# Optimization experiments

Hardware: AMD Instinct MI355X
Metric: run time of the kernel (lower is better)

The kernel has to match this reference:

```python
import jax, jax.numpy as jnp
import numpy as np

NUM_HEADS = 8


def setup_inputs() -> dict:
    key = jax.random.key(0)
    ks = jax.random.split(key, 7)
    B, D, N = 16, 512, 2048
    sc = 1.0 / np.sqrt(D)
    return {
        "X_Query": jax.random.normal(ks[0], (B, D, N), jnp.float32),
        "X_Key": jax.random.normal(ks[1], (B, D, N), jnp.float32),
        "X_Value": jax.random.normal(ks[2], (B, D, N), jnp.float32),
        "W_q": jax.random.normal(ks[3], (D, D), jnp.float32) * sc,
        "W_k": jax.random.normal(ks[4], (D, D), jnp.float32) * sc,
        "W_v": jax.random.normal(ks[5], (D, D), jnp.float32) * sc,
        "W_o": jax.random.normal(ks[6], (D, D), jnp.float32) * sc,
    }


def _proj(W, x):
    # Conv1d(D, D, kernel_size=1, bias=False) == channel matmul
    return jnp.einsum('oi,bin->bon', W, x)


def _split_heads(x, h):
    # torch: cat(x.chunk(h, dim=-1), dim=0) -> (h, B, D, N/h) stacked layout
    B, D, N = x.shape
    return x.reshape(B, D, h, N // h).transpose(2, 0, 1, 3)


def _mha(XQ, XK, XV, Wq, Wk, Wv, Wo):
    B, D, N = XQ.shape
    h = NUM_HEADS
    Nh = N // h
    q = _split_heads(_proj(Wq, XQ), h)  # (h, B, D, Nh)
    k = _split_heads(_proj(Wk, XK), h)
    v = _split_heads(_proj(Wv, XV), h)
    # scores over the CHANNEL axis: (h, B, D, D), scaled by sqrt(d_k)=sqrt(Nh)
    scores = jnp.einsum('hbdn,hben->hbde', q, k) / jnp.sqrt(jnp.asarray(Nh, q.dtype))
    p = jax.nn.softmax(scores, axis=-1)
    out = jnp.einsum('hbde,hben->hbdn', p, v)  # (h, B, D, Nh)
    # torch: cat(chunks, dim=0) inverse -> cat along dim=-1
    attn_heads = out.transpose(1, 2, 0, 3).reshape(B, D, N)
    return _proj(Wo, XQ - attn_heads)


def reference(X_Query, X_Key, X_Value, W_q, W_k, W_v, W_o):
    return _mha(X_Query, X_Key, X_Value, W_q, W_k, W_v, W_o)
```

## Files before the change

kernel.cpp:

```cpp
#include <hip/hip_runtime.h>
#include <hip/hip_bf16.h>

#define DD  512
#define NN  2048
#define BB  16
#define NHD 256

typedef unsigned short u16;
typedef __attribute__((ext_vector_type(4))) float f32x4;
typedef __attribute__((ext_vector_type(8))) short s16x8;
typedef __attribute__((ext_vector_type(4))) u16   u16x4;

static __device__ __forceinline__ u16 f2bf(float f) {
  __hip_bfloat16 h = __float2bfloat16(f);
  return *reinterpret_cast<u16*>(&h);
}
static __device__ __forceinline__ float bf2f(u16 u) {
  union { unsigned int i; float f; } v; v.i = ((unsigned int)u) << 16; return v.f;
}
static __device__ __forceinline__ f32x4 mfma_bf16(s16x8 a, s16x8 b, f32x4 c) {
  return __builtin_amdgcn_mfma_f32_16x16x32_bf16(a, b, c, 0, 0, 0);
}
static __device__ __forceinline__ void gload_lds16(const u16* g, u16* l) {
  __builtin_amdgcn_global_load_lds(
      (const __attribute__((address_space(1))) unsigned int*)g,
      (__attribute__((address_space(3))) unsigned int*)l, 16, 0, 0);
}

__global__ __launch_bounds__(256) void k_cvt_w(const float* __restrict__ w0,
                                               const float* __restrict__ w1,
                                               const float* __restrict__ w2,
                                               const float* __restrict__ w3,
                                               u16* __restrict__ out) {
  const float* srcs[4] = {w0, w1, w2, w3};
  const float* s = srcs[blockIdx.y];
  u16* o = out + (size_t)blockIdx.y * (DD * DD);
  int idx = blockIdx.x * 256 + threadIdx.x;
  float4 v = *(const float4*)(s + (size_t)idx * 4);
  u16x4 u = {f2bf(v.x), f2bf(v.y), f2bf(v.z), f2bf(v.w)};
  *(u16x4*)(o + (size_t)idx * 4) = u;
}

__global__ __launch_bounds__(256) void k_transpose(const float* __restrict__ X,
                                                   u16* __restrict__ XT) {
  __shared__ float t[64][68];
  const int tid = threadIdx.x;
  const int n0 = blockIdx.x * 64, d0 = blockIdx.y * 64, b = blockIdx.z;
  const float* Xb = X + ((size_t)b * DD + d0) * NN + n0;
#pragma unroll
  for (int i = 0; i < 4; ++i) {
    int r = (tid >> 4) + i * 16;
    int c = (tid & 15) * 4;
    float4 v = *(const float4*)(Xb + (size_t)r * NN + c);
    t[r][c] = v.x; t[r][c + 1] = v.y; t[r][c + 2] = v.z; t[r][c + 3] = v.w;
  }
  __syncthreads();
  u16* Ob = XT + ((size_t)b * NN + n0) * DD + d0;
#pragma unroll
  for (int i = 0; i < 4; ++i) {
    int n = (tid >> 4) + i * 16;
    int d = (tid & 15) * 4;
    u16x4 u = {f2bf(t[d][n]), f2bf(t[d + 1][n]), f2bf(t[d + 2][n]), f2bf(t[d + 3][n])};
    *(u16x4*)(Ob + (size_t)n * DD + d) = u;
  }
}

#define GEMM_STAGE(Ag, lda, Bg, ldb, buf, kt)                                   \
  {                                                                             \
    _Pragma("unroll")                                                           \
    for (int j = 0; j < 4; ++j) {                                               \
      int s = j * 256 + w * 64 + lane;                                          \
      int row = s >> 3, u = s & 7;                                              \
      int col = ((u ^ (row & 7)) * 8);                                          \
      gload_lds16(Ag + (size_t)row * lda + (kt) * 64 + col, &Ab[buf][s * 8]);   \
      gload_lds16(Bg + (size_t)row * ldb + (kt) * 64 + col, &Bb[buf][s * 8]);   \
    }                                                                           \
  }

#define GEMM_COMPUTE(buf)                                                       \
  {                                                                             \
    _Pragma("unroll")                                                           \
    for (int ks = 0; ks < 2; ++ks) {                                            \
      s16x8 av[4], bv[4];                                                       \
      _Pragma("unroll")                                                         \
      for (int m = 0; m < 4; ++m) {                                             \
        int row = wm + m * 16 + r;                                              \
        av[m] = *(const s16x8*)&Ab[buf][row * 64 + (((ks * 4 + g) ^ (row & 7)) * 8)]; \
      }                                                                         \
      _Pragma("unroll")                                                         \
      for (int nf = 0; nf < 4; ++nf) {                                          \
        int row = wn + nf * 16 + r;                                             \
        bv[nf] = *(const s16x8*)&Bb[buf][row * 64 + (((ks * 4 + g) ^ (row & 7)) * 8)]; \
      }                                                                         \
      _Pragma("unroll")                                                         \
      for (int m = 0; m < 4; ++m)                                               \
        _Pragma("unroll")                                                       \
        for (int nf = 0; nf < 4; ++nf)                                          \
          acc[m][nf] = mfma_bf16(av[m], bv[nf], acc[m][nf]);                    \
    }                                                                           \
  }

#define GEMM_PREAMBLE                                                           \
  __shared__ __align__(16) u16 Ab[2][128 * 64];                                 \
  __shared__ __align__(16) u16 Bb[2][128 * 64];                                 \
  const int tid = threadIdx.x;                                                  \
  const int lane = tid & 63, w = tid >> 6;                                      \
  const int wm = (w >> 1) * 64, wn = (w & 1) * 64;                              \
  const int r = lane & 15, g = lane >> 4;                                       \
  f32x4 acc[4][4] = {};

#define GEMM_MAINLOOP(Ag, lda, Bg, ldb, nkt)                                    \
  GEMM_STAGE(Ag, lda, Bg, ldb, 0, 0);                                           \
  __syncthreads();                                                              \
  for (int kt = 0; kt < (nkt) - 1; ++kt) {                                      \
    GEMM_STAGE(Ag, lda, Bg, ldb, (kt & 1) ^ 1, kt + 1);                         \
    GEMM_COMPUTE(kt & 1);                                                       \
    __syncthreads();                                                            \
  }                                                                             \
  GEMM_COMPUTE(((nkt) - 1) & 1);

template <typename OUT_T>
__global__ __launch_bounds__(256) void k_gemm_nt(
    const u16* __restrict__ A, long long a_bs, int lda,
    const u16* __restrict__ B, long long b_bs, int ldb,
    OUT_T* __restrict__ C, long long c_bs, int ldc, int K) {
  GEMM_PREAMBLE
  const int m0 = blockIdx.x * 128, n0 = blockIdx.y * 128;
  const u16* Ag = A + (size_t)blockIdx.z * a_bs + (size_t)m0 * lda;
  const u16* Bg = B + (size_t)blockIdx.z * b_bs + (size_t)n0 * ldb;
  const int nkt = K >> 6;
  GEMM_MAINLOOP(Ag, lda, Bg, ldb, nkt);

  OUT_T* Cg = C + (size_t)blockIdx.z * c_bs;
#pragma unroll
  for (int m = 0; m < 4; ++m)
#pragma unroll
    for (int nf = 0; nf < 4; ++nf)
#pragma unroll
      for (int j = 0; j < 4; ++j) {
        int row = m0 + wm + m * 16 + g * 4 + j;
        int col = n0 + wn + nf * 16 + r;
        float v = acc[m][nf][j];
        if constexpr (sizeof(OUT_T) == 2) Cg[(size_t)row * ldc + col] = f2bf(v);
        else                              Cg[(size_t)row * ldc + col] = v;
      }
}

__global__ __launch_bounds__(512, 4) void k_attn_fused(
    const u16* __restrict__ Qdn, const u16* __restrict__ Kdn,
    const u16* __restrict__ VT,  const u16* __restrict__ XqT,
    u16* __restrict__ And) {
  __shared__ __align__(16) u16 L[36864];
  u16* Ks = L;
  u16* Vs = L + 16384;
  u16* Ps = L + 32768;

  const int tid = threadIdx.x;
  const int lane = tid & 63, w = tid >> 6;
  const int r = lane & 15, g = lane >> 4;
  const int dq = w >> 1, eh = w & 1;
  const int nq = w >> 1, dh = w & 1;
  const int bid = blockIdx.x;
  const int dt = bid >> 7, hb = bid & 127;
  const int h = hb & 7, b = hb >> 3;
  const int d0 = dt * 64, hn0 = h * NHD;

  const u16* Qg = Qdn + ((size_t)b * DD + d0) * NN + hn0;
  const u16* Kg = Kdn + ((size_t)b * DD) * NN + hn0;
  const u16* Vg = VT + ((size_t)b * NN + hn0) * DD;

  auto stage_k = [&](int idx) {
    const int e0 = (idx >> 1) * 64, c0 = (idx & 1) * 128;
    u16* dst = Ks + (idx & 1) * 8192;
#pragma unroll
    for (int j = 0; j < 2; ++j) {
      int s = j * 512 + tid;
      int row = s >> 4, u = s & 15;
      gload_lds16(Kg + (size_t)(e0 + row) * NN + c0 + ((u ^ (row & 7)) * 8), dst + s * 8);
    }
  };
  auto stage_v = [&](int t) {
    u16* dst = Vs + (t & 1) * 8192;
#pragma unroll
    for (int j = 0; j < 2; ++j) {
      int s = j * 512 + tid;
      int row = s >> 2, u = s & 3;
      gload_lds16(Vg + (size_t)row * DD + t * 32 + ((u ^ ((row >> 1) & 3)) * 8), dst + s * 8);
    }
  };

  stage_k(0);
#pragma unroll
  for (int j = 0; j < 4; ++j) {
    int s = j * 512 + tid;
    int row = s >> 5, u = s & 31;
    gload_lds16(Qg + (size_t)row * NN + ((u ^ (row & 7)) * 8), Vs + s * 8);
  }
  __syncthreads();
  s16x8 qf[8];
#pragma unroll
  for (int k2 = 0; k2 < 8; ++k2) {
    int row = dq * 16 + r;
    qf[k2] = *(const s16x8*)&Vs[row * 256 + (((k2 * 4 + g) ^ (row & 7)) * 8)];
  }
  __syncthreads();

  float psum[4] = {};
  f32x4 acc_o[4][2] = {};

  for (int et = 0; et < 8; ++et) {
    f32x4 acc_s[2] = {};
#pragma unroll
    for (int nsub = 0; nsub < 2; ++nsub) {
      const int idx = et * 2 + nsub;
      if (idx + 1 < 16) stage_k(idx + 1);
      stage_v(idx);
      const u16* kb = Ks + (idx & 1) * 8192;
#pragma unroll
      for (int kq = 0; kq < 4; ++kq) {
        s16x8 bv[2];
#pragma unroll
        for (int nf = 0; nf < 2; ++nf) {
          int rowe = eh * 32 + nf * 16 + r;
          bv[nf] = *(const s16x8*)&kb[rowe * 128 + (((kq * 4 + g) ^ (rowe & 7)) * 8)];
        }
        acc_s[0] = mfma_bf16(qf[nsub * 4 + kq], bv[0], acc_s[0]);
        acc_s[1] = mfma_bf16(qf[nsub * 4 + kq], bv[1], acc_s[1]);
      }
      __syncthreads();
    }
#pragma unroll
    for (int nf = 0; nf < 2; ++nf)
#pragma unroll
      for (int j = 0; j < 4; ++j) {
        int rowd = dq * 16 + g * 4 + j;
        int cole = eh * 32 + nf * 16 + r;
        float p = __expf(acc_s[nf][j] * 0.0625f);
        psum[j] += p;
        *(u16*)((char*)Ps + rowd * 128 + (((cole >> 3) ^ (rowd & 7)) * 16) +
                (cole & 7) * 2) = f2bf(p);
      }
    __syncthreads();
#pragma unroll
    for (int vs = 0; vs < 2; ++vs) {
      s16x8 pb[2];
#pragma unroll
      for (int nf = 0; nf < 2; ++nf) {
        int rowd = dh * 32 + nf * 16 + r;
        pb[nf] = *(const s16x8*)((char*)Ps + rowd * 128 + (((vs * 4 + g) ^ (rowd & 7)) * 16));
      }
      const u16* vb = Vs + ((et * 2 + vs) & 1) * 8192;
#pragma unroll
      for (int ms = 0; ms < 4; ++ms) {
        int rown = nq * 64 + ms * 16 + r;
        s16x8 av = *(const s16x8*)&vb[rown * 32 + ((g ^ ((rown >> 1) & 3)) * 8)];
        acc_o[ms][0] = mfma_bf16(av, pb[0], acc_o[ms][0]);
        acc_o[ms][1] = mfma_bf16(av, pb[1], acc_o[ms][1]);
      }
    }
    __syncthreads();
  }

  float* rs = (float*)L;
#pragma unroll
  for (int j = 0; j < 4; ++j) {
    float v = psum[j];
    v += __shfl_xor(v, 1);
    v += __shfl_xor(v, 2);
    v += __shfl_xor(v, 4);
    v += __shfl_xor(v, 8);
    if (r == 0) rs[w * 16 + g * 4 + j] = v;
  }
  __syncthreads();
  if (tid < 64) {
    int dqi = tid >> 4, i = tid & 15;
    rs[128 + tid] = 1.0f / (rs[(dqi * 2) * 16 + i] + rs[(dqi * 2 + 1) * 16 + i]);
  }
  __syncthreads();

  const u16* Xg = XqT + ((size_t)b * NN + hn0) * DD + d0;
  u16* Ag = And + ((size_t)b * NN + hn0) * DD + d0;
#pragma unroll
  for (int ms = 0; ms < 4; ++ms)
#pragma unroll
    for (int nf = 0; nf < 2; ++nf) {
      const int cold = dh * 32 + nf * 16 + r;
      const float inv = rs[128 + cold];
#pragma unroll
      for (int j = 0; j < 4; ++j) {
        const int npos = nq * 64 + ms * 16 + g * 4 + j;
        float o = acc_o[ms][nf][j] * inv;
        float xq = bf2f(Xg[(size_t)npos * DD + cold]);
        Ag[(size_t)npos * DD + cold] = f2bf(xq - o);
      }
    }
}

extern "C" void kernel_launch(void* const* d_in, const int* in_sizes, int n_in,
                              void* d_out, int out_size, void* d_ws, size_t ws_size,
                              hipStream_t stream) {
  const float* Xq = (const float*)d_in[0];
  const float* Xk = (const float*)d_in[1];
  const float* Xv = (const float*)d_in[2];
  const float* Wq = (const float*)d_in[3];
  const float* Wk = (const float*)d_in[4];
  const float* Wv = (const float*)d_in[5];
  const float* Wo = (const float*)d_in[6];
  float* out = (float*)d_out;

  char* ws = (char*)d_ws;
  const size_t MB = 1024 * 1024;
  u16* Wb  = (u16*)ws;
  u16* XqT = (u16*)(ws + 2 * MB);
  u16* Z2  = (u16*)(ws + 34 * MB);
  u16* And = Z2;
  u16* Qdn = (u16*)(ws + 66 * MB);
  u16* VTb = (u16*)d_out;
  u16* Kdn = (u16*)d_out + (size_t)BB * NN * DD;

  k_cvt_w<<<dim3(256, 4), 256, 0, stream>>>(Wq, Wk, Wv, Wo, Wb);

  k_transpose<<<dim3(NN / 64, DD / 64, BB), 256, 0, stream>>>(Xv, Z2);
  k_gemm_nt<u16><<<dim3(NN / 128, DD / 128, BB), 256, 0, stream>>>(
      Z2, (long long)NN * DD, DD,
      Wb + 2 * DD * DD, 0, DD,
      VTb, (long long)NN * DD, DD, DD);

  k_transpose<<<dim3(NN / 64, DD / 64, BB), 256, 0, stream>>>(Xq, XqT);
  k_gemm_nt<u16><<<dim3(DD / 128, NN / 128, BB), 256, 0, stream>>>(
      Wb, 0, DD,
      XqT, (long long)NN * DD, DD,
      Qdn, (long long)DD * NN, NN, DD);

  k_transpose<<<dim3(NN / 64, DD / 64, BB), 256, 0, stream>>>(Xk, Z2);
  k_gemm_nt<u16><<<dim3(DD / 128, NN / 128, BB), 256, 0, stream>>>(
      Wb + 1 * DD * DD, 0, DD,
      Z2, (long long)NN * DD, DD,
      Kdn, (long long)DD * NN, NN, DD);

  k_attn_fused<<<dim3(1024), 512, 0, stream>>>(Qdn, Kdn, VTb, XqT, And);

  k_gemm_nt<float><<<dim3(DD / 128, NN / 128, BB), 256, 0, stream>>>(
      Wb + 3 * DD * DD, 0, DD,
      And, (long long)NN * DD, DD,
      out, (long long)DD * NN, NN, DD);
}
```

Baseline: 255.0 us.

## Replace syncthreads with explicit waitcnt and raw barriers in fused attention

Swaps the __syncthreads calls in the fused attention kernel for explicit s_waitcnt vmcnt/lgkmcnt counts plus raw s_barrier with scheduler fences. Async global-to-LDS loads for K and V can then stay in flight across barriers instead of being fully drained each time. It also changes the P tile in LDS from an XOR swizzle to padded rows (stride 72) and grows the LDS buffer to fit. The hand-written vmcnt counts must match the number of outstanding loads per thread exactly, so any miscount races, and the fixed scheduling fences limit compiler reordering.

```diff
diff --git a/kernel.cpp b/kernel.cpp
--- a/kernel.cpp
+++ b/kernel.cpp
@@ -26,6 +26,13 @@
       (const __attribute__((address_space(1))) unsigned int*)g,
       (__attribute__((address_space(3))) unsigned int*)l, 16, 0, 0);
 }
+static __device__ __forceinline__ void barrier_raw() {
+  __builtin_amdgcn_sched_barrier(0);
+  __builtin_amdgcn_s_barrier();
+  __builtin_amdgcn_sched_barrier(0);
+}
+#define WAITCNT(s) do { asm volatile("s_waitcnt " s ::: "memory"); \
+                        __builtin_amdgcn_sched_barrier(0); } while (0)
 
 __global__ __launch_bounds__(256) void k_cvt_w(const float* __restrict__ w0,
                                                const float* __restrict__ w1,
@@ -150,7 +157,7 @@
     const u16* __restrict__ Qdn, const u16* __restrict__ Kdn,
     const u16* __restrict__ VT,  const u16* __restrict__ XqT,
     u16* __restrict__ And) {
-  __shared__ __align__(16) u16 L[36864];
+  __shared__ __align__(16) u16 L[37376];
   u16* Ks = L;
   u16* Vs = L + 16384;
   u16* Ps = L + 32768;
@@ -196,14 +203,16 @@
     int row = s >> 5, u = s & 31;
     gload_lds16(Qg + (size_t)row * NN + ((u ^ (row & 7)) * 8), Vs + s * 8);
   }
-  __syncthreads();
+  WAITCNT("vmcnt(0)");
+  barrier_raw();
   s16x8 qf[8];
 #pragma unroll
   for (int k2 = 0; k2 < 8; ++k2) {
     int row = dq * 16 + r;
     qf[k2] = *(const s16x8*)&Vs[row * 256 + (((k2 * 4 + g) ^ (row & 7)) * 8)];
   }
-  __syncthreads();
+  WAITCNT("lgkmcnt(0)");
+  barrier_raw();
 
   float psum[4] = {};
   f32x4 acc_o[4][2] = {};
@@ -213,8 +222,14 @@
 #pragma unroll
     for (int nsub = 0; nsub < 2; ++nsub) {
       const int idx = et * 2 + nsub;
-      if (idx + 1 < 16) stage_k(idx + 1);
       stage_v(idx);
+      if (idx < 15) {
+        stage_k(idx + 1);
+        WAITCNT("vmcnt(4)");
+      } else {
+        WAITCNT("vmcnt(2)");
+      }
+      barrier_raw();
       const u16* kb = Ks + (idx & 1) * 8192;
 #pragma unroll
       for (int kq = 0; kq < 4; ++kq) {
@@ -227,7 +242,8 @@
         acc_s[0] = mfma_bf16(qf[nsub * 4 + kq], bv[0], acc_s[0]);
         acc_s[1] = mfma_bf16(qf[nsub * 4 + kq], bv[1], acc_s[1]);
       }
-      __syncthreads();
+      WAITCNT("lgkmcnt(0)");
+      barrier_raw();
     }
 #pragma unroll
     for (int nf = 0; nf < 2; ++nf)
@@ -237,19 +253,21 @@
         int cole = eh * 32 + nf * 16 + r;
         float p = __expf(acc_s[nf][j] * 0.0625f);
         psum[j] += p;
-        *(u16*)((char*)Ps + rowd * 128 + (((cole >> 3) ^ (rowd & 7)) * 16) +
-                (cole & 7) * 2) = f2bf(p);
-      }
-    __syncthreads();
+        Ps[rowd * 72 + cole] = f2bf(p);
+      }
+    WAITCNT("lgkmcnt(0)");
+    if (et < 7) WAITCNT("vmcnt(2)");
+    else        WAITCNT("vmcnt(0)");
+    barrier_raw();
 #pragma unroll
     for (int vs = 0; vs < 2; ++vs) {
       s16x8 pb[2];
 #pragma unroll
       for (int nf = 0; nf < 2; ++nf) {
         int rowd = dh * 32 + nf * 16 + r;
-        pb[nf] = *(const s16x8*)((char*)Ps + rowd * 128 + (((vs * 4 + g) ^ (rowd & 7)) * 16));
-      }
-      const u16* vb = Vs + ((et * 2 + vs) & 1) * 8192;
+        pb[nf] = *(const s16x8*)&Ps[rowd * 72 + vs * 32 + g * 8];
+      }
+      const u16* vb = Vs + vs * 8192;
 #pragma unroll
       for (int ms = 0; ms < 4; ++ms) {
         int rown = nq * 64 + ms * 16 + r;
@@ -258,7 +276,8 @@
         acc_o[ms][1] = mfma_bf16(av, pb[1], acc_o[ms][1]);
       }
     }
-    __syncthreads();
+    WAITCNT("lgkmcnt(0)");
+    barrier_raw();
   }
 
   float* rs = (float*)L;
```

Measured after the change: 254.2 us. No clear change (-0.3%).
